# Performance work log

Hardware: AMD Instinct MI355X
Metric: run time of the kernel (lower is better)

Reference implementation:

```python
import jax, jax.numpy as jnp
import numpy as np

B = 8192
ALPHA, BETA, GAMMA = 1.0, 1.0, 1.0  # loss_weights alpha (MSE), beta (MR), gamma (SIM)
MR_BIAS = 0.1
COS_EPS = 1e-8  # torch F.cosine_similarity denominator clamp


def setup_inputs() -> dict:
    key = jax.random.key(0)
    k1, k2 = jax.random.split(key)
    predictions = jax.random.normal(k1, (B,), dtype=jnp.float32)
    correct_output = jax.random.normal(k2, (B,), dtype=jnp.float32)
    return {"predictions": predictions, "correct_output": correct_output}


def reference(predictions, correct_output):
    # MSE (use_confidence=False -> plain mean)
    mse = jnp.mean(jnp.square(predictions - correct_output))

    # Margin-ranking loss, vectorized over all (m, n) pairs.
    # r = sign(pred_m - pred_n) if nonzero, else -sign(gt_m - gt_n)
    dp = predictions[:, None] - predictions[None, :]        # [B, B]
    dg = correct_output[:, None] - correct_output[None, :]  # [B, B]
    r = jnp.where(dp != 0, jnp.sign(dp), -jnp.sign(dg))
    mr = jnp.mean(jnp.maximum(0.0, MR_BIAS - r * dp))

    # SIM loss: 1 - cosine similarity of the full prediction / target vectors
    dot = jnp.dot(predictions, correct_output)
    denom = jnp.maximum(jnp.linalg.norm(predictions) * jnp.linalg.norm(correct_output), COS_EPS)
    sim = 1.0 - dot / denom

    loss = ALPHA * mse + BETA * mr + GAMMA * sim
    return jnp.reshape(loss, (1,))  # torch returns shape (1,) via cosine_similarity on dim=1
```

## Files before the change

### kernel.cpp

```cpp
#include <hip/hip_runtime.h>


#define B_N 8192
#define THREADS 256
#define M_PER_THREAD 2
#define MB (THREADS * M_PER_THREAD)
#define NXB (B_N / MB)
#define CHUNK 128
#define NYB (B_N / CHUNK)
#define NBLOCKS (NXB * NYB)

__device__ __forceinline__ float block_reduce_sum(float v, float* sbuf) {
    #pragma unroll
    for (int off = 32; off > 0; off >>= 1)
        v += __shfl_down(v, off, 64);
    const int lane = threadIdx.x & 63;
    const int wave = threadIdx.x >> 6;
    if (lane == 0) sbuf[wave] = v;
    __syncthreads();
    if (threadIdx.x == 0) {
        float s = 0.f;
        #pragma unroll
        for (int w = 0; w < THREADS / 64; ++w) s += sbuf[w];
        sbuf[0] = s;
    }
    __syncthreads();
    const float r = sbuf[0];
    __syncthreads();
    return r;
}

__global__ void __launch_bounds__(THREADS)
pairwise_kernel(const float* __restrict__ p, const float* __restrict__ g,
                float* __restrict__ pairPartial,
                float* __restrict__ linPartial) {
    __shared__ float s_n[CHUNK];
    __shared__ float sbuf[THREADS / 64];

    const int tid = threadIdx.x;
    const int bx = blockIdx.x, by = blockIdx.y;
    const int m0 = bx * MB + tid;
    const int m1 = m0 + THREADS;

    if (tid < CHUNK) s_n[tid] = p[by * CHUNK + tid];
    const float pm0 = p[m0];
    const float pm1 = p[m1];
    __syncthreads();

    float a00 = 0.f, a01 = 0.f, a02 = 0.f, a03 = 0.f;
    float a10 = 0.f, a11 = 0.f, a12 = 0.f, a13 = 0.f;
    const float4* s4 = (const float4*)s_n;
    #pragma unroll 4
    for (int j = 0; j < CHUNK / 4; ++j) {
        const float4 v = s4[j];
        a00 += fmaxf(0.f, 0.1f - fabsf(pm0 - v.x));
        a01 += fmaxf(0.f, 0.1f - fabsf(pm0 - v.y));
        a02 += fmaxf(0.f, 0.1f - fabsf(pm0 - v.z));
        a03 += fmaxf(0.f, 0.1f - fabsf(pm0 - v.w));
        a10 += fmaxf(0.f, 0.1f - fabsf(pm1 - v.x));
        a11 += fmaxf(0.f, 0.1f - fabsf(pm1 - v.y));
        a12 += fmaxf(0.f, 0.1f - fabsf(pm1 - v.z));
        a13 += fmaxf(0.f, 0.1f - fabsf(pm1 - v.w));
    }
    const float acc = ((a00 + a01) + (a02 + a03)) + ((a10 + a11) + (a12 + a13));
    const float s = block_reduce_sum(acc, sbuf);
    if (tid == 0) pairPartial[by * NXB + bx] = s;

    if (by == 0) {
        const float gv0 = g[m0], gv1 = g[m1];
        const float d0 = pm0 - gv0, d1 = pm1 - gv1;
        float sq  = d0 * d0 + d1 * d1;
        float dot = pm0 * gv0 + pm1 * gv1;
        float npp = pm0 * pm0 + pm1 * pm1;
        float ngg = gv0 * gv0 + gv1 * gv1;
        sq  = block_reduce_sum(sq, sbuf);
        dot = block_reduce_sum(dot, sbuf);
        npp = block_reduce_sum(npp, sbuf);
        ngg = block_reduce_sum(ngg, sbuf);
        if (tid == 0) {
            linPartial[bx * 4 + 0] = sq;
            linPartial[bx * 4 + 1] = dot;
            linPartial[bx * 4 + 2] = npp;
            linPartial[bx * 4 + 3] = ngg;
        }
    }
}

__global__ void __launch_bounds__(THREADS)
finalize_kernel(const float* __restrict__ pairPartial,
                const float* __restrict__ linPartial,
                float* __restrict__ out) {
    __shared__ float sbuf[THREADS / 64];

    float mr = 0.f;
    #pragma unroll
    for (int k = 0; k < NBLOCKS / THREADS; ++k)
        mr += pairPartial[k * THREADS + threadIdx.x];
    mr = block_reduce_sum(mr, sbuf);

    float lv[4];
    #pragma unroll
    for (int k = 0; k < 4; ++k) {
        float v = 0.f;
        if (threadIdx.x < NXB) v = linPartial[threadIdx.x * 4 + k];
        lv[k] = block_reduce_sum(v, sbuf);
    }

    if (threadIdx.x == 0) {
        const float mse = lv[0] / (float)B_N;
        const float mrm = mr / ((float)B_N * (float)B_N);
        const float denom = fmaxf(sqrtf(lv[2]) * sqrtf(lv[3]), 1e-8f);
        const float sim = 1.f - lv[1] / denom;
        out[0] = mse + mrm + sim;
    }
}

extern "C" void kernel_launch(void* const* d_in, const int* in_sizes, int n_in,
                              void* d_out, int out_size, void* d_ws, size_t ws_size,
                              hipStream_t stream) {
    const float* p = (const float*)d_in[0];
    const float* g = (const float*)d_in[1];
    float* pairPartial = (float*)d_ws;
    float* linPartial  = (float*)d_ws + NBLOCKS;

    dim3 grid(NXB, NYB);
    pairwise_kernel<<<grid, THREADS, 0, stream>>>(p, g, pairPartial, linPartial);
    finalize_kernel<<<1, THREADS, 0, stream>>>(pairPartial, linPartial, (float*)d_out);
}
```

Measured before the change: 15.63 us.

## Exploit pair symmetry and use packed fp16 math for off-diagonal tiles

Computes only the upper triangle of the pairwise margin matrix: blocks below the diagonal exit early and write zero, diagonal tiles use strict upper-triangle loops in fp32, and the finalize step doubles the sum and adds the diagonal term. Off-diagonal tiles switch to packed half-precision arithmetic with fp16 accumulators to double ALU throughput. This roughly halves the pairwise work, but fp16 rounding of inputs and fp16 accumulation introduce precision error that may exceed tolerance. The diagonal tiles also become load-imbalanced because their loops are triangular.

After: 21.65 us. 38.6% more time.

```diff
diff --git a/kernel.cpp b/kernel.cpp
--- a/kernel.cpp
+++ b/kernel.cpp
@@ -9,6 +9,8 @@
 #define CHUNK 128
 #define NYB (B_N / CHUNK)
 #define NBLOCKS (NXB * NYB)
+
+typedef _Float16 h2 __attribute__((ext_vector_type(2)));
 
 __device__ __forceinline__ float block_reduce_sum(float v, float* sbuf) {
     #pragma unroll
@@ -34,44 +36,30 @@
 pairwise_kernel(const float* __restrict__ p, const float* __restrict__ g,
                 float* __restrict__ pairPartial,
                 float* __restrict__ linPartial) {
-    __shared__ float s_n[CHUNK];
-    __shared__ float sbuf[THREADS / 64];
+    __shared__ float    s_f[CHUNK];
+    __shared__ _Float16 s_h[CHUNK];
+    __shared__ float    sbuf[THREADS / 64];
 
     const int tid = threadIdx.x;
     const int bx = blockIdx.x, by = blockIdx.y;
+    const bool below = (by < 4 * bx);
+
+    if (below && by != 0) {
+        if (tid == 0) pairPartial[by * NXB + bx] = 0.f;
+        return;
+    }
+
     const int m0 = bx * MB + tid;
     const int m1 = m0 + THREADS;
-
-    if (tid < CHUNK) s_n[tid] = p[by * CHUNK + tid];
-    const float pm0 = p[m0];
-    const float pm1 = p[m1];
-    __syncthreads();
-
-    float a00 = 0.f, a01 = 0.f, a02 = 0.f, a03 = 0.f;
-    float a10 = 0.f, a11 = 0.f, a12 = 0.f, a13 = 0.f;
-    const float4* s4 = (const float4*)s_n;
-    #pragma unroll 4
-    for (int j = 0; j < CHUNK / 4; ++j) {
-        const float4 v = s4[j];
-        a00 += fmaxf(0.f, 0.1f - fabsf(pm0 - v.x));
-        a01 += fmaxf(0.f, 0.1f - fabsf(pm0 - v.y));
-        a02 += fmaxf(0.f, 0.1f - fabsf(pm0 - v.z));
-        a03 += fmaxf(0.f, 0.1f - fabsf(pm0 - v.w));
-        a10 += fmaxf(0.f, 0.1f - fabsf(pm1 - v.x));
-        a11 += fmaxf(0.f, 0.1f - fabsf(pm1 - v.y));
-        a12 += fmaxf(0.f, 0.1f - fabsf(pm1 - v.z));
-        a13 += fmaxf(0.f, 0.1f - fabsf(pm1 - v.w));
-    }
-    const float acc = ((a00 + a01) + (a02 + a03)) + ((a10 + a11) + (a12 + a13));
-    const float s = block_reduce_sum(acc, sbuf);
-    if (tid == 0) pairPartial[by * NXB + bx] = s;
+    const float pm0f = p[m0];
+    const float pm1f = p[m1];
 
     if (by == 0) {
         const float gv0 = g[m0], gv1 = g[m1];
-        const float d0 = pm0 - gv0, d1 = pm1 - gv1;
+        const float d0 = pm0f - gv0, d1 = pm1f - gv1;
         float sq  = d0 * d0 + d1 * d1;
-        float dot = pm0 * gv0 + pm1 * gv1;
-        float npp = pm0 * pm0 + pm1 * pm1;
+        float dot = pm0f * gv0 + pm1f * gv1;
+        float npp = pm0f * pm0f + pm1f * pm1f;
         float ngg = gv0 * gv0 + gv1 * gv1;
         sq  = block_reduce_sum(sq, sbuf);
         dot = block_reduce_sum(dot, sbuf);
@@ -84,6 +72,54 @@
             linPartial[bx * 4 + 3] = ngg;
         }
     }
+
+    if (below) {
+        if (tid == 0) pairPartial[by * NXB + bx] = 0.f;
+        return;
+    }
+
+    const int n0 = by * CHUNK;
+    if (tid < CHUNK) {
+        const float v = p[n0 + tid];
+        s_f[tid] = v;
+        s_h[tid] = (_Float16)v;
+    }
+    __syncthreads();
+
+    float pairsum;
+    if (by >= 4 * bx + 4) {
+        const h2* s2 = (const h2*)s_h;
+        const _Float16 pm0s = (_Float16)pm0f;
+        const _Float16 pm1s = (_Float16)pm1f;
+        const h2 pm0 = {pm0s, pm0s};
+        const h2 pm1 = {pm1s, pm1s};
+        const h2 bias = {(_Float16)0.1f, (_Float16)0.1f};
+        const h2 zero = {(_Float16)0.f, (_Float16)0.f};
+        h2 a0a = zero, a0b = zero, a1a = zero, a1b = zero;
+        #pragma unroll 8
+        for (int j = 0; j < CHUNK / 2; j += 2) {
+            const h2 va = s2[j];
+            const h2 vb = s2[j + 1];
+            a0a += __builtin_elementwise_max(bias - __builtin_elementwise_abs(pm0 - va), zero);
+            a0b += __builtin_elementwise_max(bias - __builtin_elementwise_abs(pm0 - vb), zero);
+            a1a += __builtin_elementwise_max(bias - __builtin_elementwise_abs(pm1 - va), zero);
+            a1b += __builtin_elementwise_max(bias - __builtin_elementwise_abs(pm1 - vb), zero);
+        }
+        const h2 s01 = (a0a + a0b) + (a1a + a1b);
+        pairsum = (float)s01.x + (float)s01.y;
+    } else {
+        float a0 = 0.f, a1 = 0.f;
+        const int js0 = max(0, m0 - n0 + 1);
+        for (int j = js0; j < CHUNK; ++j)
+            a0 += fmaxf(0.f, 0.1f - fabsf(pm0f - s_f[j]));
+        const int js1 = max(0, m1 - n0 + 1);
+        for (int j = js1; j < CHUNK; ++j)
+            a1 += fmaxf(0.f, 0.1f - fabsf(pm1f - s_f[j]));
+        pairsum = a0 + a1;
+    }
+
+    const float s = block_reduce_sum(pairsum, sbuf);
+    if (tid == 0) pairPartial[by * NXB + bx] = s;
 }
 
 __global__ void __launch_bounds__(THREADS)
@@ -92,11 +128,11 @@
                 float* __restrict__ out) {
     __shared__ float sbuf[THREADS / 64];
 
-    float mr = 0.f;
+    float tri = 0.f;
     #pragma unroll
     for (int k = 0; k < NBLOCKS / THREADS; ++k)
-        mr += pairPartial[k * THREADS + threadIdx.x];
-    mr = block_reduce_sum(mr, sbuf);
+        tri += pairPartial[k * THREADS + threadIdx.x];
+    tri = block_reduce_sum(tri, sbuf);
 
     float lv[4];
     #pragma unroll
@@ -108,7 +144,8 @@
 
     if (threadIdx.x == 0) {
         const float mse = lv[0] / (float)B_N;
-        const float mrm = mr / ((float)B_N * (float)B_N);
+        const float mr_total = 2.f * tri + 0.1f * (float)B_N;
+        const float mrm = mr_total / ((float)B_N * (float)B_N);
         const float denom = fmaxf(sqrtf(lv[2]) * sqrtf(lv[3]), 1e-8f);
         const float sim = 1.f - lv[1] / denom;
         out[0] = mse + mrm + sim;
```
